# Performance work log

Measured on AMD Instinct MI355X. Metric: run time of the kernel, lower is better.

Reference implementation:

```python
import jax, jax.numpy as jnp
import numpy as np

EMB_SIZE = 768
NUM_HEADS = 8


def setup_inputs() -> dict:
    key = jax.random.key(0)
    ks = jax.random.split(key, 6)
    B, N, E = 8, 1024, EMB_SIZE
    return {
        "x": jax.random.normal(ks[0], (B, N, E), dtype=jnp.float32),
        "relative_pos": jax.random.normal(ks[1], (NUM_HEADS, N, N), dtype=jnp.float32),
        "qkv_w": jax.random.normal(ks[2], (2 * E, E), dtype=jnp.float32) * 0.02,
        "qkv_b": jax.random.normal(ks[3], (2 * E,), dtype=jnp.float32) * 0.02,
        "val_w": jax.random.normal(ks[4], (E, E), dtype=jnp.float32) * 0.02,
        "val_b": jax.random.normal(ks[5], (E,), dtype=jnp.float32) * 0.02,
    }


def reference(x, relative_pos, qkv_w, qkv_b, val_w, val_b):
    B, N, E = x.shape
    H = NUM_HEADS
    D = E // H
    # qkv projection: [B, N, 2E]; last dim layout is (h, d, qk) per einops rearrange
    qkv = (x @ qkv_w.T + qkv_b).reshape(B, N, H, D, 2)
    q = jnp.transpose(qkv[..., 0], (0, 2, 1, 3))  # [B, H, N, D]
    k = jnp.transpose(qkv[..., 1], (0, 2, 1, 3))  # [B, H, N, D]
    scale = E ** 0.5  # original divides by sqrt(emb_size), not sqrt(d_head)
    energy = jnp.einsum('bhqd,bhkd->bhqk', q, k) / scale  # [B, H, N, N]
    # relative_pos [H, N, N] broadcasts over batch
    energy = jax.nn.softmax(energy + relative_pos, axis=-1)
    values = x @ val_w.T + val_b  # [B, N, E]
    return values, energy
```

## Files before the change

### kernel.cpp

```cpp
#include <hip/hip_runtime.h>
#include <hip/hip_bf16.h>

#define EMB 768
#define NH 8
#define DH 96
#define BATCH 8
#define SEQ 1024
#define M_TOT (BATCH * SEQ)
#define NCOLS (3 * EMB)

typedef float f32x4 __attribute__((ext_vector_type(4)));
typedef __bf16 bf16x8 __attribute__((ext_vector_type(8)));

__device__ __forceinline__ unsigned short f2bf_bits(float f) {
  __hip_bfloat16 b = __float2bfloat16(f);
  return *reinterpret_cast<unsigned short*>(&b);
}

__device__ __forceinline__ void gload_lds16(const void* g, void* l) {
  __builtin_amdgcn_global_load_lds(
      (__attribute__((address_space(1))) void*)(g),
      (__attribute__((address_space(3))) void*)(l), 16, 0, 0);
}

__global__ void prep_x_kernel(const float* __restrict__ x, __hip_bfloat16* __restrict__ xb) {
  const int n4 = M_TOT * EMB / 4;
  int i = blockIdx.x * blockDim.x + threadIdx.x;
  if (i < n4) {
    f32x4 v = reinterpret_cast<const f32x4*>(x)[i];
    ushort4 o;
    o.x = f2bf_bits(v[0]);
    o.y = f2bf_bits(v[1]);
    o.z = f2bf_bits(v[2]);
    o.w = f2bf_bits(v[3]);
    reinterpret_cast<ushort4*>(xb)[i] = o;
  }
}

__global__ void prep_w_kernel(const float* __restrict__ qkv_w, const float* __restrict__ qkv_b,
                              const float* __restrict__ val_w, const float* __restrict__ val_b,
                              __hip_bfloat16* __restrict__ Wall, float* __restrict__ bias) {
  const float inv_s = 0.03608439182435161f;
  int idx = blockIdx.x * 256 + threadIdx.x;
  if (idx >= NCOLS * EMB) return;
  int r = idx / EMB;
  int c = idx - r * EMB;
  float v;
  if (r < EMB) {
    int h = r / DH, d = r - h * DH;
    int src = h * 192 + 2 * d;
    v = qkv_w[(size_t)src * EMB + c] * inv_s;
    if (c == 0) bias[r] = qkv_b[src] * inv_s;
  } else if (r < 2 * EMB) {
    int r2 = r - EMB;
    int h = r2 / DH, d = r2 - h * DH;
    int src = h * 192 + 2 * d + 1;
    v = qkv_w[(size_t)src * EMB + c];
    if (c == 0) bias[r] = qkv_b[src];
  } else {
    int r3 = r - 2 * EMB;
    v = val_w[(size_t)r3 * EMB + c];
    if (c == 0) bias[r] = val_b[r3];
  }
  Wall[idx] = __float2bfloat16(v);
}

__global__ __launch_bounds__(256) void gemm_kernel(
    const __hip_bfloat16* __restrict__ xb, const __hip_bfloat16* __restrict__ Wall,
    const float* __restrict__ bias, __hip_bfloat16* __restrict__ qhead,
    __hip_bfloat16* __restrict__ khead, float* __restrict__ vout) {
  __shared__ __hip_bfloat16 As[128 * 32];
  __shared__ __hip_bfloat16 Bs[128 * 32];
  __shared__ __hip_bfloat16 Cs[128][136];
  const int tid = threadIdx.x;
  const int w = tid >> 6, l = tid & 63;
  const int m0 = blockIdx.x * 128;
  const int n0 = blockIdx.y * 128;
  const int wr = w >> 1, wc = w & 1;

  f32x4 acc[4][4] = {};

  const int sr0 = (w * 2 + 0) * 16 + (l >> 2);
  const int sr1 = (w * 2 + 1) * 16 + (l >> 2);
  const int sc = (l & 3) * 8;

  for (int kt = 0; kt < EMB / 32; ++kt) {
    const int k0 = kt * 32;
    gload_lds16(xb + (size_t)(m0 + sr0) * EMB + k0 + sc, (void*)(As + (w * 2 + 0) * 512));
    gload_lds16(xb + (size_t)(m0 + sr1) * EMB + k0 + sc, (void*)(As + (w * 2 + 1) * 512));
    gload_lds16(Wall + (size_t)(n0 + sr0) * EMB + k0 + sc, (void*)(Bs + (w * 2 + 0) * 512));
    gload_lds16(Wall + (size_t)(n0 + sr1) * EMB + k0 + sc, (void*)(Bs + (w * 2 + 1) * 512));
    __syncthreads();

    bf16x8 af[4], bfr[4];
#pragma unroll
    for (int t = 0; t < 4; ++t) {
      af[t] = *reinterpret_cast<const bf16x8*>(As + (wr * 64 + t * 16 + (l & 15)) * 32 + (l >> 4) * 8);
      bfr[t] = *reinterpret_cast<const bf16x8*>(Bs + (wc * 64 + t * 16 + (l & 15)) * 32 + (l >> 4) * 8);
    }
#pragma unroll
    for (int i = 0; i < 4; ++i)
#pragma unroll
      for (int j = 0; j < 4; ++j)
        acc[i][j] = __builtin_amdgcn_mfma_f32_16x16x32_bf16(af[i], bfr[j], acc[i][j], 0, 0, 0);
    __syncthreads();
  }

  if (n0 >= 2 * EMB) {
    const int rowbase = m0 + wr * 64;
    const int colbase = n0 - 2 * EMB + wc * 64;
#pragma unroll
    for (int j = 0; j < 4; ++j) {
      const int n = colbase + j * 16 + (l & 15);
      const float bb = bias[2 * EMB + n];
#pragma unroll
      for (int i = 0; i < 4; ++i) {
#pragma unroll
        for (int q = 0; q < 4; ++q) {
          const int m = rowbase + i * 16 + (l >> 4) * 4 + q;
          vout[(size_t)m * EMB + n] = acc[i][j][q] + bb;
        }
      }
    }
  } else {
#pragma unroll
    for (int j = 0; j < 4; ++j) {
      const int nl = wc * 64 + j * 16 + (l & 15);
      const float bb = bias[n0 + nl];
#pragma unroll
      for (int i = 0; i < 4; ++i) {
#pragma unroll
        for (int q = 0; q < 4; ++q) {
          const int ml = wr * 64 + i * 16 + (l >> 4) * 4 + q;
          Cs[ml][nl] = __float2bfloat16(acc[i][j][q] + bb);
        }
      }
    }
    __syncthreads();
    __hip_bfloat16* dst = (n0 >= EMB) ? khead : qhead;
    const int ch0 = (n0 >= EMB) ? (n0 - EMB) : n0;
    const int cg = (tid & 15) * 8;
    const int gch = ch0 + cg;
    const int hh = gch / DH, dd = gch - hh * DH;
#pragma unroll
    for (int pass = 0; pass < 8; ++pass) {
      const int r = pass * 16 + (tid >> 4);
      const int m = m0 + r;
      const int bb_ = m >> 10, mm = m & 1023;
      bf16x8 v8 = *reinterpret_cast<const bf16x8*>(&Cs[r][cg]);
      *reinterpret_cast<bf16x8*>(dst + ((size_t)(bb_ * NH + hh) * SEQ + mm) * DH + dd) = v8;
    }
  }
}

__global__ __launch_bounds__(512, 2) void attn_kernel(
    const __hip_bfloat16* __restrict__ qhead, const __hip_bfloat16* __restrict__ khead,
    const float* __restrict__ rel, float* __restrict__ eout) {
  __shared__ alignas(16) char KS[8 * 3 * 3072];
  __shared__ float redm[16][8];
  __shared__ float reds[16][8];

  const int t = threadIdx.x;
  const int w = t >> 6, l = t & 63;
  const int lr = l >> 4, lc = l & 15;
  const int flat = blockIdx.x;
  const int u = flat >> 6;
  const int b = (flat >> 3) & 7;
  const int g = u * 8 + (flat & 7);
  const int h = g >> 6;
  const int rb = g & 63;
  const int row0 = rb * 16;
  const size_t bh = (size_t)(b * NH + h);

  const __hip_bfloat16* qsrc = qhead + (bh * SEQ + row0 + lc) * DH;
  bf16x8 qf[3];
#pragma unroll
  for (int kc = 0; kc < 3; ++kc)
    qf[kc] = *reinterpret_cast<const bf16x8*>(qsrc + kc * 32 + lr * 8);

  const float* relsrc = rel + ((size_t)h * SEQ + row0 + lc) * SEQ + w * 128 + lr * 4;
  f32x4 relv[8];
#pragma unroll
  for (int s = 0; s < 8; ++s)
    relv[s] = *reinterpret_cast<const f32x4*>(relsrc + s * 16);

  const __hip_bfloat16* ksrc = khead + bh * SEQ * DH + (size_t)w * 128 * DH;
  char* kdst = KS + w * 9216;

#define STAGE_K(s, buf)                                                             \
  {                                                                                 \
    const __hip_bfloat16* s_ = ksrc + (size_t)(s) * 1536 + (size_t)l * 8;           \
    gload_lds16(s_, kdst + (buf) * 3072);                                           \
    gload_lds16(s_ + 512, kdst + (buf) * 3072 + 1024);                              \
    gload_lds16(s_ + 1024, kdst + (buf) * 3072 + 2048);                             \
  }

  STAGE_K(0, 0)
  STAGE_K(1, 1)

  f32x4 acc[8];
#pragma unroll
  for (int s = 0; s < 8; ++s) {
    if (s < 6) STAGE_K(s + 2, (s + 2) % 3)
    if (s < 6) {
      asm volatile("s_waitcnt vmcnt(6)" ::: "memory");
    } else if (s == 6) {
      asm volatile("s_waitcnt vmcnt(3)" ::: "memory");
    } else {
      asm volatile("s_waitcnt vmcnt(0)" ::: "memory");
    }
    __builtin_amdgcn_sched_barrier(0);
    const __hip_bfloat16* kp =
        reinterpret_cast<const __hip_bfloat16*>(kdst + (s % 3) * 3072) + lc * DH;
    f32x4 a = {0.f, 0.f, 0.f, 0.f};
    __builtin_amdgcn_s_setprio(1);
#pragma unroll
    for (int kc = 0; kc < 3; ++kc) {
      bf16x8 kf = *reinterpret_cast<const bf16x8*>(kp + kc * 32 + lr * 8);
      a = __builtin_amdgcn_mfma_f32_16x16x32_bf16(kf, qf[kc], a, 0, 0, 0);
    }
    __builtin_amdgcn_s_setprio(0);
    acc[s] = a + relv[s];
  }
#undef STAGE_K

  float mx = -3.4e38f;
#pragma unroll
  for (int s = 0; s < 8; ++s)
    mx = fmaxf(mx, fmaxf(fmaxf(acc[s][0], acc[s][1]), fmaxf(acc[s][2], acc[s][3])));
  mx = fmaxf(mx, __shfl_xor(mx, 16));
  mx = fmaxf(mx, __shfl_xor(mx, 32));
  if (l < 16) redm[lc][w] = mx;
  __syncthreads();
  float M = redm[lc][0];
#pragma unroll
  for (int i = 1; i < 8; ++i) M = fmaxf(M, redm[lc][i]);

  float sm = 0.f;
#pragma unroll
  for (int s = 0; s < 8; ++s) {
#pragma unroll
    for (int j = 0; j < 4; ++j) {
      float e = __expf(acc[s][j] - M);
      acc[s][j] = e;
      sm += e;
    }
  }
  sm += __shfl_xor(sm, 16);
  sm += __shfl_xor(sm, 32);
  if (l < 16) reds[lc][w] = sm;
  __syncthreads();
  float S = 0.f;
#pragma unroll
  for (int i = 0; i < 8; ++i) S += reds[lc][i];
  const float rinv = 1.0f / S;

  float* op = eout + (bh * SEQ + row0 + lc) * SEQ + w * 128 + lr * 4;
#pragma unroll
  for (int s = 0; s < 8; ++s) {
    f32x4 v = acc[s] * rinv;
    __builtin_nontemporal_store(v, reinterpret_cast<f32x4*>(op + s * 16));
  }
}

extern "C" void kernel_launch(void* const* d_in, const int* in_sizes, int n_in,
                              void* d_out, int out_size, void* d_ws, size_t ws_size,
                              hipStream_t stream) {
  const float* x = (const float*)d_in[0];
  const float* rel = (const float*)d_in[1];
  const float* qkv_w = (const float*)d_in[2];
  const float* qkv_b = (const float*)d_in[3];
  const float* val_w = (const float*)d_in[4];
  const float* val_b = (const float*)d_in[5];
  float* out = (float*)d_out;

  char* ws = (char*)d_ws;
  __hip_bfloat16* xb = (__hip_bfloat16*)(ws);
  __hip_bfloat16* Wall = (__hip_bfloat16*)(ws + 12582912);
  float* bias = (float*)(ws + 16121856);
  __hip_bfloat16* qhead = (__hip_bfloat16*)(ws + 16131072);
  __hip_bfloat16* khead = (__hip_bfloat16*)(ws + 28713984);

  float* vout = out;
  float* eout = out + (size_t)M_TOT * EMB;

  prep_x_kernel<<<dim3(M_TOT * EMB / 4 / 256), dim3(256), 0, stream>>>(x, xb);
  prep_w_kernel<<<dim3(NCOLS * EMB / 256), dim3(256), 0, stream>>>(qkv_w, qkv_b, val_w, val_b,
                                                                   Wall, bias);
  gemm_kernel<<<dim3(M_TOT / 128, NCOLS / 128), dim3(256), 0, stream>>>(xb, Wall, bias, qhead,
                                                                        khead, vout);
  attn_kernel<<<dim3(SEQ / 16 * NH * BATCH), dim3(512), 0, stream>>>(qhead, khead, rel, eout);
}
```

Measured before the change: 161.1 us.

## Transpose attention scores through LDS for row-contiguous rel loads and output stores

The attention kernel now writes MFMA accumulator tiles to LDS with an XOR swizzle, reusing the K staging buffer, and reads them back so each half-wave owns 512 contiguous bytes of one row. The relative_pos loads and the energy stores therefore become fully coalesced row segments instead of 16-byte pieces scattered over 16 rows. Row max and sum reductions change to 5-step shuffles per row for 8 rows per lane. The value-projection epilogue also switches to nontemporal stores. The cost is an extra LDS round trip and more shuffle work in exchange for better global memory access patterns.

```diff
diff --git a/kernel.cpp b/kernel.cpp
--- a/kernel.cpp
+++ b/kernel.cpp
@@ -118,7 +118,7 @@
 #pragma unroll
         for (int q = 0; q < 4; ++q) {
           const int m = rowbase + i * 16 + (l >> 4) * 4 + q;
-          vout[(size_t)m * EMB + n] = acc[i][j][q] + bb;
+          __builtin_nontemporal_store(acc[i][j][q] + bb, &vout[(size_t)m * EMB + n]);
         }
       }
     }
@@ -163,6 +163,7 @@
   const int t = threadIdx.x;
   const int w = t >> 6, l = t & 63;
   const int lr = l >> 4, lc = l & 15;
+  const int rl = l >> 5, cl = l & 31;
   const int flat = blockIdx.x;
   const int u = flat >> 6;
   const int b = (flat >> 3) & 7;
@@ -178,11 +179,11 @@
   for (int kc = 0; kc < 3; ++kc)
     qf[kc] = *reinterpret_cast<const bf16x8*>(qsrc + kc * 32 + lr * 8);
 
-  const float* relsrc = rel + ((size_t)h * SEQ + row0 + lc) * SEQ + w * 128 + lr * 4;
+  const float* relsrc = rel + ((size_t)h * SEQ + row0 + rl) * SEQ + w * 128 + cl * 4;
   f32x4 relv[8];
 #pragma unroll
-  for (int s = 0; s < 8; ++s)
-    relv[s] = *reinterpret_cast<const f32x4*>(relsrc + s * 16);
+  for (int i = 0; i < 8; ++i)
+    relv[i] = *reinterpret_cast<const f32x4*>(relsrc + (size_t)(2 * i) * SEQ);
 
   const __hip_bfloat16* ksrc = khead + bh * SEQ * DH + (size_t)w * 128 * DH;
   char* kdst = KS + w * 9216;
@@ -197,6 +198,7 @@
 
   STAGE_K(0, 0)
   STAGE_K(1, 1)
+  __builtin_amdgcn_sched_barrier(0);
 
   f32x4 acc[8];
 #pragma unroll
@@ -220,46 +222,77 @@
       a = __builtin_amdgcn_mfma_f32_16x16x32_bf16(kf, qf[kc], a, 0, 0, 0);
     }
     __builtin_amdgcn_s_setprio(0);
-    acc[s] = a + relv[s];
+    acc[s] = a;
   }
 #undef STAGE_K
-
-  float mx = -3.4e38f;
+  asm volatile("s_waitcnt lgkmcnt(0)" ::: "memory");
+  __builtin_amdgcn_sched_barrier(0);
+
 #pragma unroll
   for (int s = 0; s < 8; ++s)
-    mx = fmaxf(mx, fmaxf(fmaxf(acc[s][0], acc[s][1]), fmaxf(acc[s][2], acc[s][3])));
-  mx = fmaxf(mx, __shfl_xor(mx, 16));
-  mx = fmaxf(mx, __shfl_xor(mx, 32));
-  if (l < 16) redm[lc][w] = mx;
+    *reinterpret_cast<f32x4*>(kdst + lc * 512 + ((s * 64 + lr * 16) ^ ((lc & 7) << 4))) =
+        acc[s];
+  asm volatile("s_waitcnt lgkmcnt(0)" ::: "memory");
+  __builtin_amdgcn_sched_barrier(0);
+  f32x4 v[8];
+#pragma unroll
+  for (int i = 0; i < 8; ++i) {
+    const int r = 2 * i + rl;
+    v[i] = *reinterpret_cast<const f32x4*>(kdst + r * 512 + ((cl * 16) ^ ((r & 7) << 4)));
+  }
+
+#pragma unroll
+  for (int i = 0; i < 8; ++i) v[i] = v[i] + relv[i];
+
+  float mx[8];
+#pragma unroll
+  for (int i = 0; i < 8; ++i)
+    mx[i] = fmaxf(fmaxf(v[i][0], v[i][1]), fmaxf(v[i][2], v[i][3]));
+#pragma unroll
+  for (int d = 1; d < 32; d <<= 1)
+#pragma unroll
+    for (int i = 0; i < 8; ++i) mx[i] = fmaxf(mx[i], __shfl_xor(mx[i], d));
+  if (cl == 0) {
+#pragma unroll
+    for (int i = 0; i < 8; ++i) redm[2 * i + rl][w] = mx[i];
+  }
   __syncthreads();
-  float M = redm[lc][0];
-#pragma unroll
-  for (int i = 1; i < 8; ++i) M = fmaxf(M, redm[lc][i]);
-
-  float sm = 0.f;
-#pragma unroll
-  for (int s = 0; s < 8; ++s) {
-#pragma unroll
-    for (int j = 0; j < 4; ++j) {
-      float e = __expf(acc[s][j] - M);
-      acc[s][j] = e;
-      sm += e;
-    }
-  }
-  sm += __shfl_xor(sm, 16);
-  sm += __shfl_xor(sm, 32);
-  if (l < 16) reds[lc][w] = sm;
+  float M[8];
+#pragma unroll
+  for (int i = 0; i < 8; ++i) {
+    const float* rm = redm[2 * i + rl];
+    M[i] = fmaxf(fmaxf(fmaxf(rm[0], rm[1]), fmaxf(rm[2], rm[3])),
+                 fmaxf(fmaxf(rm[4], rm[5]), fmaxf(rm[6], rm[7])));
+  }
+
+  float sm[8];
+#pragma unroll
+  for (int i = 0; i < 8; ++i) {
+    f32x4 e;
+    e[0] = __expf(v[i][0] - M[i]);
+    e[1] = __expf(v[i][1] - M[i]);
+    e[2] = __expf(v[i][2] - M[i]);
+    e[3] = __expf(v[i][3] - M[i]);
+    v[i] = e;
+    sm[i] = (e[0] + e[1]) + (e[2] + e[3]);
+  }
+#pragma unroll
+  for (int d = 1; d < 32; d <<= 1)
+#pragma unroll
+    for (int i = 0; i < 8; ++i) sm[i] += __shfl_xor(sm[i], d);
+  if (cl == 0) {
+#pragma unroll
+    for (int i = 0; i < 8; ++i) reds[2 * i + rl][w] = sm[i];
+  }
   __syncthreads();
-  float S = 0.f;
-#pragma unroll
-  for (int i = 0; i < 8; ++i) S += reds[lc][i];
-  const float rinv = 1.0f / S;
-
-  float* op = eout + (bh * SEQ + row0 + lc) * SEQ + w * 128 + lr * 4;
-#pragma unroll
-  for (int s = 0; s < 8; ++s) {
-    f32x4 v = acc[s] * rinv;
-    __builtin_nontemporal_store(v, reinterpret_cast<f32x4*>(op + s * 16));
+
+  float* op = eout + (bh * SEQ + row0 + rl) * SEQ + w * 128 + cl * 4;
+#pragma unroll
+  for (int i = 0; i < 8; ++i) {
+    const float* rs = reds[2 * i + rl];
+    const float S = ((rs[0] + rs[1]) + (rs[2] + rs[3])) + ((rs[4] + rs[5]) + (rs[6] + rs[7]));
+    f32x4 vv = v[i] * (1.0f / S);
+    __builtin_nontemporal_store(vv, reinterpret_cast<f32x4*>(op + (size_t)(2 * i) * SEQ));
   }
 }
 
```

Result: slower. 168.6 us (+4.7%).

## Process 32 query rows per attention block to reuse staged K tiles

Applied to the files above, without the earlier changes.

Each attention block now handles two 16-row query tiles instead of one, so every K tile staged into LDS feeds two MFMA chains. This halves the grid size and the total K global-to-LDS traffic. The relative-position bias is now prefetched one step ahead inside the loop instead of all at once, with the vmcnt waits adjusted to match. Launch bounds are raised to 4 blocks per CU to trim register pressure, which risks spills given the doubled accumulators.

```diff
diff --git a/kernel.cpp b/kernel.cpp
--- a/kernel.cpp
+++ b/kernel.cpp
@@ -153,12 +153,12 @@
   }
 }
 
-__global__ __launch_bounds__(512, 2) void attn_kernel(
+__global__ __launch_bounds__(512, 4) void attn_kernel(
     const __hip_bfloat16* __restrict__ qhead, const __hip_bfloat16* __restrict__ khead,
     const float* __restrict__ rel, float* __restrict__ eout) {
   __shared__ alignas(16) char KS[8 * 3 * 3072];
-  __shared__ float redm[16][8];
-  __shared__ float reds[16][8];
+  __shared__ float redm[32][8];
+  __shared__ float reds[32][8];
 
   const int t = threadIdx.x;
   const int w = t >> 6, l = t & 63;
@@ -167,22 +167,24 @@
   const int u = flat >> 6;
   const int b = (flat >> 3) & 7;
   const int g = u * 8 + (flat & 7);
-  const int h = g >> 6;
-  const int rb = g & 63;
-  const int row0 = rb * 16;
+  const int h = g >> 5;
+  const int rb = g & 31;
+  const int row0 = rb * 32;
   const size_t bh = (size_t)(b * NH + h);
 
   const __hip_bfloat16* qsrc = qhead + (bh * SEQ + row0 + lc) * DH;
-  bf16x8 qf[3];
-#pragma unroll
-  for (int kc = 0; kc < 3; ++kc)
-    qf[kc] = *reinterpret_cast<const bf16x8*>(qsrc + kc * 32 + lr * 8);
-
-  const float* relsrc = rel + ((size_t)h * SEQ + row0 + lc) * SEQ + w * 128 + lr * 4;
-  f32x4 relv[8];
-#pragma unroll
-  for (int s = 0; s < 8; ++s)
-    relv[s] = *reinterpret_cast<const f32x4*>(relsrc + s * 16);
+  bf16x8 qf1[3], qf2[3];
+#pragma unroll
+  for (int kc = 0; kc < 3; ++kc) {
+    qf1[kc] = *reinterpret_cast<const bf16x8*>(qsrc + kc * 32 + lr * 8);
+    qf2[kc] = *reinterpret_cast<const bf16x8*>(qsrc + 16 * DH + kc * 32 + lr * 8);
+  }
+
+  const float* rel1 = rel + ((size_t)h * SEQ + row0 + lc) * SEQ + w * 128 + lr * 4;
+  const float* rel2 = rel1 + 16 * SEQ;
+  f32x4 rc1 = *reinterpret_cast<const f32x4*>(rel1);
+  f32x4 rc2 = *reinterpret_cast<const f32x4*>(rel2);
+  __builtin_amdgcn_sched_barrier(0);
 
   const __hip_bfloat16* ksrc = khead + bh * SEQ * DH + (size_t)w * 128 * DH;
   char* kdst = KS + w * 9216;
@@ -197,69 +199,109 @@
 
   STAGE_K(0, 0)
   STAGE_K(1, 1)
-
-  f32x4 acc[8];
+  __builtin_amdgcn_sched_barrier(0);
+
+  f32x4 acc1[8], acc2[8];
 #pragma unroll
   for (int s = 0; s < 8; ++s) {
+    f32x4 rn1 = {}, rn2 = {};
+    if (s < 7) {
+      rn1 = *reinterpret_cast<const f32x4*>(rel1 + (s + 1) * 16);
+      rn2 = *reinterpret_cast<const f32x4*>(rel2 + (s + 1) * 16);
+    }
+    __builtin_amdgcn_sched_barrier(0);
     if (s < 6) STAGE_K(s + 2, (s + 2) % 3)
+    __builtin_amdgcn_sched_barrier(0);
     if (s < 6) {
-      asm volatile("s_waitcnt vmcnt(6)" ::: "memory");
+      asm volatile("s_waitcnt vmcnt(8)" ::: "memory");
     } else if (s == 6) {
-      asm volatile("s_waitcnt vmcnt(3)" ::: "memory");
+      asm volatile("s_waitcnt vmcnt(5)" ::: "memory");
     } else {
       asm volatile("s_waitcnt vmcnt(0)" ::: "memory");
     }
     __builtin_amdgcn_sched_barrier(0);
     const __hip_bfloat16* kp =
         reinterpret_cast<const __hip_bfloat16*>(kdst + (s % 3) * 3072) + lc * DH;
-    f32x4 a = {0.f, 0.f, 0.f, 0.f};
+    f32x4 a1 = {0.f, 0.f, 0.f, 0.f};
+    f32x4 a2 = {0.f, 0.f, 0.f, 0.f};
     __builtin_amdgcn_s_setprio(1);
 #pragma unroll
     for (int kc = 0; kc < 3; ++kc) {
       bf16x8 kf = *reinterpret_cast<const bf16x8*>(kp + kc * 32 + lr * 8);
-      a = __builtin_amdgcn_mfma_f32_16x16x32_bf16(kf, qf[kc], a, 0, 0, 0);
+      a1 = __builtin_amdgcn_mfma_f32_16x16x32_bf16(kf, qf1[kc], a1, 0, 0, 0);
+      a2 = __builtin_amdgcn_mfma_f32_16x16x32_bf16(kf, qf2[kc], a2, 0, 0, 0);
     }
     __builtin_amdgcn_s_setprio(0);
-    acc[s] = a + relv[s];
+    acc1[s] = a1 + rc1;
+    acc2[s] = a2 + rc2;
+    if (s < 7) {
+      rc1 = rn1;
+      rc2 = rn2;
+    }
   }
 #undef STAGE_K
 
-  float mx = -3.4e38f;
-#pragma unroll
-  for (int s = 0; s < 8; ++s)
-    mx = fmaxf(mx, fmaxf(fmaxf(acc[s][0], acc[s][1]), fmaxf(acc[s][2], acc[s][3])));
-  mx = fmaxf(mx, __shfl_xor(mx, 16));
-  mx = fmaxf(mx, __shfl_xor(mx, 32));
-  if (l < 16) redm[lc][w] = mx;
+  float mx1 = -3.4e38f, mx2 = -3.4e38f;
+#pragma unroll
+  for (int s = 0; s < 8; ++s) {
+    mx1 = fmaxf(mx1, fmaxf(fmaxf(acc1[s][0], acc1[s][1]), fmaxf(acc1[s][2], acc1[s][3])));
+    mx2 = fmaxf(mx2, fmaxf(fmaxf(acc2[s][0], acc2[s][1]), fmaxf(acc2[s][2], acc2[s][3])));
+  }
+  mx1 = fmaxf(mx1, __shfl_xor(mx1, 16));
+  mx1 = fmaxf(mx1, __shfl_xor(mx1, 32));
+  mx2 = fmaxf(mx2, __shfl_xor(mx2, 16));
+  mx2 = fmaxf(mx2, __shfl_xor(mx2, 32));
+  if (l < 16) {
+    redm[lc][w] = mx1;
+    redm[16 + lc][w] = mx2;
+  }
   __syncthreads();
-  float M = redm[lc][0];
-#pragma unroll
-  for (int i = 1; i < 8; ++i) M = fmaxf(M, redm[lc][i]);
-
-  float sm = 0.f;
+  float M1 = redm[lc][0], M2 = redm[16 + lc][0];
+#pragma unroll
+  for (int i = 1; i < 8; ++i) {
+    M1 = fmaxf(M1, redm[lc][i]);
+    M2 = fmaxf(M2, redm[16 + lc][i]);
+  }
+
+  float sm1 = 0.f, sm2 = 0.f;
 #pragma unroll
   for (int s = 0; s < 8; ++s) {
 #pragma unroll
     for (int j = 0; j < 4; ++j) {
-      float e = __expf(acc[s][j] - M);
-      acc[s][j] = e;
-      sm += e;
-    }
-  }
-  sm += __shfl_xor(sm, 16);
-  sm += __shfl_xor(sm, 32);
-  if (l < 16) reds[lc][w] = sm;
+      float e1 = __expf(acc1[s][j] - M1);
+      float e2 = __expf(acc2[s][j] - M2);
+      acc1[s][j] = e1;
+      acc2[s][j] = e2;
+      sm1 += e1;
+      sm2 += e2;
+    }
+  }
+  sm1 += __shfl_xor(sm1, 16);
+  sm1 += __shfl_xor(sm1, 32);
+  sm2 += __shfl_xor(sm2, 16);
+  sm2 += __shfl_xor(sm2, 32);
+  if (l < 16) {
+    reds[lc][w] = sm1;
+    reds[16 + lc][w] = sm2;
+  }
   __syncthreads();
-  float S = 0.f;
-#pragma unroll
-  for (int i = 0; i < 8; ++i) S += reds[lc][i];
-  const float rinv = 1.0f / S;
-
-  float* op = eout + (bh * SEQ + row0 + lc) * SEQ + w * 128 + lr * 4;
+  float S1 = 0.f, S2 = 0.f;
+#pragma unroll
+  for (int i = 0; i < 8; ++i) {
+    S1 += reds[lc][i];
+    S2 += reds[16 + lc][i];
+  }
+  const float rinv1 = 1.0f / S1;
+  const float rinv2 = 1.0f / S2;
+
+  float* op1 = eout + (bh * SEQ + row0 + lc) * SEQ + w * 128 + lr * 4;
+  float* op2 = op1 + 16 * SEQ;
 #pragma unroll
   for (int s = 0; s < 8; ++s) {
-    f32x4 v = acc[s] * rinv;
-    __builtin_nontemporal_store(v, reinterpret_cast<f32x4*>(op + s * 16));
+    f32x4 v1 = acc1[s] * rinv1;
+    f32x4 v2 = acc2[s] * rinv2;
+    __builtin_nontemporal_store(v1, reinterpret_cast<f32x4*>(op1 + s * 16));
+    __builtin_nontemporal_store(v2, reinterpret_cast<f32x4*>(op2 + s * 16));
   }
 }
 
@@ -289,5 +331,5 @@
                                                                    Wall, bias);
   gemm_kernel<<<dim3(M_TOT / 128, NCOLS / 128), dim3(256), 0, stream>>>(xb, Wall, bias, qhead,
                                                                         khead, vout);
-  attn_kernel<<<dim3(SEQ / 16 * NH * BATCH), dim3(512), 0, stream>>>(qhead, khead, rel, eout);
-}
+  attn_kernel<<<dim3(SEQ / 32 * NH * BATCH), dim3(512), 0, stream>>>(qhead, khead, rel, eout);
+}
```

Result: slower. 164.7 us (+2.2%).

## Move value projection GEMM into attention kernel as extra blocks

Applied to the files above, without the earlier changes.

The value-projection part of the combined GEMM (columns 2E..3E) is removed from the QKV GEMM launch, which now covers only the Q and K columns. It is computed instead by 384 extra blocks appended to the attention launch. Those blocks use only the first 256 of their 512 threads. The aim is to shorten the GEMM critical path and let the value GEMM fill idle CUs alongside the memory-bound softmax blocks. The cost is half-idle thread blocks, a larger unified shared-memory footprint, and a launch_bounds change to 4 that may constrain registers in the attention path.

```diff
diff --git a/kernel.cpp b/kernel.cpp
--- a/kernel.cpp
+++ b/kernel.cpp
@@ -106,64 +106,111 @@
     __syncthreads();
   }
 
-  if (n0 >= 2 * EMB) {
-    const int rowbase = m0 + wr * 64;
-    const int colbase = n0 - 2 * EMB + wc * 64;
-#pragma unroll
-    for (int j = 0; j < 4; ++j) {
-      const int n = colbase + j * 16 + (l & 15);
-      const float bb = bias[2 * EMB + n];
-#pragma unroll
-      for (int i = 0; i < 4; ++i) {
-#pragma unroll
-        for (int q = 0; q < 4; ++q) {
-          const int m = rowbase + i * 16 + (l >> 4) * 4 + q;
-          vout[(size_t)m * EMB + n] = acc[i][j][q] + bb;
+#pragma unroll
+  for (int j = 0; j < 4; ++j) {
+    const int nl = wc * 64 + j * 16 + (l & 15);
+    const float bb = bias[n0 + nl];
+#pragma unroll
+    for (int i = 0; i < 4; ++i) {
+#pragma unroll
+      for (int q = 0; q < 4; ++q) {
+        const int ml = wr * 64 + i * 16 + (l >> 4) * 4 + q;
+        Cs[ml][nl] = __float2bfloat16(acc[i][j][q] + bb);
+      }
+    }
+  }
+  __syncthreads();
+  __hip_bfloat16* dst = (n0 >= EMB) ? khead : qhead;
+  const int ch0 = (n0 >= EMB) ? (n0 - EMB) : n0;
+  const int cg = (tid & 15) * 8;
+  const int gch = ch0 + cg;
+  const int hh = gch / DH, dd = gch - hh * DH;
+#pragma unroll
+  for (int pass = 0; pass < 8; ++pass) {
+    const int r = pass * 16 + (tid >> 4);
+    const int m = m0 + r;
+    const int bb_ = m >> 10, mm = m & 1023;
+    bf16x8 v8 = *reinterpret_cast<const bf16x8*>(&Cs[r][cg]);
+    *reinterpret_cast<bf16x8*>(dst + ((size_t)(bb_ * NH + hh) * SEQ + mm) * DH + dd) = v8;
+  }
+}
+
+__global__ __launch_bounds__(512, 4) void attn_v_kernel(
+    const __hip_bfloat16* __restrict__ qhead, const __hip_bfloat16* __restrict__ khead,
+    const float* __restrict__ rel, float* __restrict__ eout,
+    const __hip_bfloat16* __restrict__ xb, const __hip_bfloat16* __restrict__ Wall,
+    const float* __restrict__ bias, float* __restrict__ vout) {
+  __shared__ alignas(16) char SM[74752];
+  const int t = threadIdx.x;
+  const int flat = blockIdx.x;
+
+  if (flat >= 4096) {
+    __hip_bfloat16* As = (__hip_bfloat16*)SM;
+    __hip_bfloat16* Bs = (__hip_bfloat16*)(SM + 8192);
+    const int vb = flat - 4096;
+    const int m0 = (vb & 63) * 128;
+    const int nv0 = (vb >> 6) * 128;
+    const int w = t >> 6, l = t & 63;
+    const int wr = w >> 1, wc = w & 1;
+    const int sr0 = (w * 2 + 0) * 16 + (l >> 2);
+    const int sr1 = (w * 2 + 1) * 16 + (l >> 2);
+    const int sc = (l & 3) * 8;
+
+    f32x4 acc[4][4] = {};
+    for (int kt = 0; kt < EMB / 32; ++kt) {
+      const int k0 = kt * 32;
+      if (t < 256) {
+        gload_lds16(xb + (size_t)(m0 + sr0) * EMB + k0 + sc, (void*)(As + (w * 2 + 0) * 512));
+        gload_lds16(xb + (size_t)(m0 + sr1) * EMB + k0 + sc, (void*)(As + (w * 2 + 1) * 512));
+        gload_lds16(Wall + (size_t)(2 * EMB + nv0 + sr0) * EMB + k0 + sc,
+                    (void*)(Bs + (w * 2 + 0) * 512));
+        gload_lds16(Wall + (size_t)(2 * EMB + nv0 + sr1) * EMB + k0 + sc,
+                    (void*)(Bs + (w * 2 + 1) * 512));
+      }
+      __syncthreads();
+      if (t < 256) {
+        bf16x8 af[4], bfr[4];
+#pragma unroll
+        for (int tt = 0; tt < 4; ++tt) {
+          af[tt] =
+              *reinterpret_cast<const bf16x8*>(As + (wr * 64 + tt * 16 + (l & 15)) * 32 + (l >> 4) * 8);
+          bfr[tt] =
+              *reinterpret_cast<const bf16x8*>(Bs + (wc * 64 + tt * 16 + (l & 15)) * 32 + (l >> 4) * 8);
+        }
+#pragma unroll
+        for (int i = 0; i < 4; ++i)
+#pragma unroll
+          for (int j = 0; j < 4; ++j)
+            acc[i][j] = __builtin_amdgcn_mfma_f32_16x16x32_bf16(af[i], bfr[j], acc[i][j], 0, 0, 0);
+      }
+      __syncthreads();
+    }
+    if (t < 256) {
+      const int rowbase = m0 + wr * 64;
+      const int colbase = nv0 + wc * 64;
+#pragma unroll
+      for (int j = 0; j < 4; ++j) {
+        const int n = colbase + j * 16 + (l & 15);
+        const float bb = bias[2 * EMB + n];
+#pragma unroll
+        for (int i = 0; i < 4; ++i) {
+#pragma unroll
+          for (int q = 0; q < 4; ++q) {
+            const int m = rowbase + i * 16 + (l >> 4) * 4 + q;
+            vout[(size_t)m * EMB + n] = acc[i][j][q] + bb;
+          }
         }
       }
     }
-  } else {
-#pragma unroll
-    for (int j = 0; j < 4; ++j) {
-      const int nl = wc * 64 + j * 16 + (l & 15);
-      const float bb = bias[n0 + nl];
-#pragma unroll
-      for (int i = 0; i < 4; ++i) {
-#pragma unroll
-        for (int q = 0; q < 4; ++q) {
-          const int ml = wr * 64 + i * 16 + (l >> 4) * 4 + q;
-          Cs[ml][nl] = __float2bfloat16(acc[i][j][q] + bb);
-        }
-      }
-    }
-    __syncthreads();
-    __hip_bfloat16* dst = (n0 >= EMB) ? khead : qhead;
-    const int ch0 = (n0 >= EMB) ? (n0 - EMB) : n0;
-    const int cg = (tid & 15) * 8;
-    const int gch = ch0 + cg;
-    const int hh = gch / DH, dd = gch - hh * DH;
-#pragma unroll
-    for (int pass = 0; pass < 8; ++pass) {
-      const int r = pass * 16 + (tid >> 4);
-      const int m = m0 + r;
-      const int bb_ = m >> 10, mm = m & 1023;
-      bf16x8 v8 = *reinterpret_cast<const bf16x8*>(&Cs[r][cg]);
-      *reinterpret_cast<bf16x8*>(dst + ((size_t)(bb_ * NH + hh) * SEQ + mm) * DH + dd) = v8;
-    }
-  }
-}
-
-__global__ __launch_bounds__(512, 2) void attn_kernel(
-    const __hip_bfloat16* __restrict__ qhead, const __hip_bfloat16* __restrict__ khead,
-    const float* __restrict__ rel, float* __restrict__ eout) {
-  __shared__ alignas(16) char KS[8 * 3 * 3072];
-  __shared__ float redm[16][8];
-  __shared__ float reds[16][8];
-
-  const int t = threadIdx.x;
+    return;
+  }
+
+  char* KS = SM;
+  float(*redm)[8] = (float(*)[8])(SM + 73728);
+  float(*reds)[8] = (float(*)[8])(SM + 74240);
+
   const int w = t >> 6, l = t & 63;
   const int lr = l >> 4, lc = l & 15;
-  const int flat = blockIdx.x;
   const int u = flat >> 6;
   const int b = (flat >> 3) & 7;
   const int g = u * 8 + (flat & 7);
@@ -287,7 +334,8 @@
   prep_x_kernel<<<dim3(M_TOT * EMB / 4 / 256), dim3(256), 0, stream>>>(x, xb);
   prep_w_kernel<<<dim3(NCOLS * EMB / 256), dim3(256), 0, stream>>>(qkv_w, qkv_b, val_w, val_b,
                                                                    Wall, bias);
-  gemm_kernel<<<dim3(M_TOT / 128, NCOLS / 128), dim3(256), 0, stream>>>(xb, Wall, bias, qhead,
-                                                                        khead, vout);
-  attn_kernel<<<dim3(SEQ / 16 * NH * BATCH), dim3(512), 0, stream>>>(qhead, khead, rel, eout);
-}
+  gemm_kernel<<<dim3(M_TOT / 128, 12), dim3(256), 0, stream>>>(xb, Wall, bias, qhead, khead,
+                                                               vout);
+  attn_v_kernel<<<dim3(4096 + 384), dim3(512), 0, stream>>>(qhead, khead, rel, eout, xb, Wall,
+                                                            bias, vout);
+}
```

Measured after the change: 162.5 us. Within noise of the previous version (+0.8%).
